# Kernel optimization log

Hardware: AMD Instinct MI355X
Metric: run time of the kernel (lower is better)

Reference implementation:

```python
import jax, jax.numpy as jnp
import numpy as np

B, L, H, NH = 8, 256, 128, 4
D = H // NH
NEG = jnp.float32(-(2.0 ** 32) + 1.0)


def setup_inputs() -> dict:
    key = jax.random.key(0)
    ks = jax.random.split(key, 12)
    f = lambda k, s, sc=1.0: jax.random.normal(k, s, dtype=jnp.float32) * sc
    inp = {
        "queries": f(ks[0], (B, L, H)),
        "keys": f(ks[1], (B, L, H)),
        "time_matrix_K": f(ks[2], (B, L, L, H), 0.05),
        "time_matrix_V": f(ks[3], (B, L, L, H), 0.05),
        "abs_pos_K": f(ks[4], (B, L, H), 0.1),
        "abs_pos_V": f(ks[5], (B, L, H), 0.1),
        "Wq": f(ks[6], (H, H), 1.0 / np.sqrt(H)),
        "bq": jnp.zeros((H,), jnp.float32),
        "Wk": f(ks[7], (H, H), 1.0 / np.sqrt(H)),
        "bk": jnp.zeros((H,), jnp.float32),
        "Wv": f(ks[8], (H, H), 1.0 / np.sqrt(H)),
        "bv": jnp.zeros((H,), jnp.float32),
        # True = padded query row (masked out)
        "time_mask": jax.random.uniform(ks[9], (B, L)) < 0.1,
        # causal mask: True above the diagonal = not attendable
        "attn_mask": jnp.triu(jnp.ones((L, L), dtype=bool), k=1),
    }
    return inp


def reference(queries, keys, time_matrix_K, time_matrix_V, abs_pos_K, abs_pos_V,
              Wq, bq, Wk, bk, Wv, bv, time_mask, attn_mask):
    # Linear projections (torch Linear: x @ W.T + b)
    Q = queries @ Wq.T + bq
    K = keys @ Wk.T + bk
    V = keys @ Wv.T + bv
    # head split: channels [i*D:(i+1)*D] -> head i  (equivalent to torch split/cat)
    Qh = Q.reshape(B, L, NH, D)
    Kh = K.reshape(B, L, NH, D)
    Vh = V.reshape(B, L, NH, D)
    pKh = abs_pos_K.reshape(B, L, NH, D)
    pVh = abs_pos_V.reshape(B, L, NH, D)
    tKh = time_matrix_K.reshape(B, L, L, NH, D)
    tVh = time_matrix_V.reshape(B, L, L, NH, D)
    # scores: QK^T + Q*absposK^T + per-row time-interval bias  -> [B,NH,L,L]
    aw = jnp.einsum('blhd,bmhd->bhlm', Qh, Kh)
    aw += jnp.einsum('blhd,bmhd->bhlm', Qh, pKh)
    aw += jnp.einsum('blmhd,blhd->bhlm', tKh, Qh)
    aw = aw * jnp.float32(1.0 / np.sqrt(D))
    mask = time_mask[:, None, :, None] | attn_mask[None, None, :, :]
    aw = jnp.where(mask, NEG, aw)
    A = jax.nn.softmax(aw, axis=-1)  # dropout omitted (eval mode)
    # outputs: A@V + A@absposV + per-row A @ time_matrix_V  -> [B,L,NH,D]
    out = jnp.einsum('bhlm,bmhd->blhd', A, Vh)
    out += jnp.einsum('bhlm,bmhd->blhd', A, pVh)
    out += jnp.einsum('bhlm,blmhd->blhd', A, tVh)
    return out.reshape(B, L, H)
```

## Files before the change

kernel.cpp:

```cpp
#include <hip/hip_runtime.h>
#include <math.h>

#define Bdim 8
#define Lq   256
#define Hd   128

static constexpr float kNEG = -4294967295.0f;
static constexpr float kScale = 0.17677669529663687f;
static constexpr float kUni = 0.00390625f;

__global__ __launch_bounds__(256) void prep_kernel(
    const float* __restrict__ Wq, const float* __restrict__ Wk,
    const float* __restrict__ Wv, const unsigned char* __restrict__ raw,
    float* __restrict__ Wt, int* __restrict__ outmask)
{
    const int blk = blockIdx.x;
    if (blk < 12) {
        __shared__ float tile[64][65];
        const int mi = blk >> 2;
        const float* W = (mi == 0) ? Wq : (mi == 1) ? Wk : Wv;
        float* WT = Wt + mi * (Hd * Hd);
        const int ti = blk & 3;
        const int r0 = (ti >> 1) * 64, c0 = (ti & 1) * 64;
        #pragma unroll
        for (int k = 0; k < 16; ++k) {
            const int e = threadIdx.x + k * 256;
            const int r = e >> 6, c = e & 63;
            tile[r][c] = W[(r0 + r) * Hd + (c0 + c)];
        }
        __syncthreads();
        #pragma unroll
        for (int k = 0; k < 16; ++k) {
            const int e = threadIdx.x + k * 256;
            const int r = e >> 6, c = e & 63;
            WT[(c0 + r) * Hd + (r0 + c)] = tile[c][r];
        }
    } else {
        __shared__ int cnt;
        if (threadIdx.x == 0) cnt = 0;
        __syncthreads();
        const int n = Bdim * Lq;
        for (int i = threadIdx.x; i < n; i += 256)
            if ((i & 3) && raw[i]) atomicAdd(&cnt, 1);
        __syncthreads();
        const bool is_u8 = (cnt > 0);
        const int* raw32 = (const int*)raw;
        for (int i = threadIdx.x; i < n; i += 256) {
            const int v = is_u8 ? (int)raw[i] : raw32[i];
            outmask[i] = (v != 0) ? 1 : 0;
        }
    }
}

__global__ __launch_bounds__(512) void proj_kernel(
    const float* __restrict__ queries, const float* __restrict__ keys,
    const float* __restrict__ absK, const float* __restrict__ absV,
    const float* __restrict__ Wt,
    const float* __restrict__ bq, const float* __restrict__ bk,
    const float* __restrict__ bv,
    float* __restrict__ Qb, float* __restrict__ Kb, float* __restrict__ Vb)
{
    constexpr int R = 8;
    __shared__ float xq[R][Hd];
    __shared__ float xk[R][Hd];
    const int row0 = blockIdx.x * R;
    const int tid = threadIdx.x;
    #pragma unroll
    for (int k = 0; k < 2; ++k) {
        const int e = tid + k * 512;
        const int r = e >> 7, c = e & 127;
        xq[r][c] = queries[(row0 + r) * Hd + c];
        xk[r][c] = keys[(row0 + r) * Hd + c];
    }
    __syncthreads();

    const int o = tid & 127, rh = tid >> 7;
    const int r0 = rh * 2, r1 = rh * 2 + 1;
    const float* __restrict__ Wtq = Wt;
    const float* __restrict__ Wtk = Wt + Hd * Hd;
    const float* __restrict__ Wtv = Wt + 2 * Hd * Hd;

    float qa0 = bq[o], qa1 = qa0;
    float ka0 = bk[o] + absK[(row0 + r0) * Hd + o];
    float ka1 = bk[o] + absK[(row0 + r1) * Hd + o];
    float va0 = bv[o] + absV[(row0 + r0) * Hd + o];
    float va1 = bv[o] + absV[(row0 + r1) * Hd + o];

    #pragma unroll 4
    for (int i = 0; i < Hd; ++i) {
        const float wq = Wtq[i * Hd + o];
        const float wk = Wtk[i * Hd + o];
        const float wv = Wtv[i * Hd + o];
        const float x0 = xq[r0][i], x1 = xq[r1][i];
        const float y0 = xk[r0][i], y1 = xk[r1][i];
        qa0 += x0 * wq; qa1 += x1 * wq;
        ka0 += y0 * wk; ka1 += y1 * wk;
        va0 += y0 * wv; va1 += y1 * wv;
    }
    Qb[(row0 + r0) * Hd + o] = qa0;  Qb[(row0 + r1) * Hd + o] = qa1;
    Kb[(row0 + r0) * Hd + o] = ka0;  Kb[(row0 + r1) * Hd + o] = ka1;
    Vb[(row0 + r0) * Hd + o] = va0;  Vb[(row0 + r1) * Hd + o] = va1;
}

__global__ __launch_bounds__(256) void attn_kernel(
    const float* __restrict__ Qb, const float* __restrict__ Kb,
    const float* __restrict__ Vb,
    const float* __restrict__ tK, const float* __restrict__ tV,
    const int* __restrict__ tmask, float* __restrict__ out)
{
    const int bid = blockIdx.x;
    const int b  = bid & 7;
    const int hp = (bid >> 3) & 1;
    const int j  = bid >> 4;

    const int tid = threadIdx.x;
    const int w = tid >> 6;
    const int h = hp * 2 + (w & 1);
    const int p = j * 2 + (w >> 1);
    const int l0 = p;
    const int l1 = 255 - p;
    const int m_off = (tid >> 2) & 15;
    const int cg = tid & 3;
    const int ch = h * 32 + cg * 8;

    const float* q0b = Qb + ((size_t)b * Lq + l0) * Hd + ch;
    const float* q1b = Qb + ((size_t)b * Lq + l1) * Hd + ch;
    float4 q00 = ((const float4*)q0b)[0], q01 = ((const float4*)q0b)[1];
    float4 q10 = ((const float4*)q1b)[0], q11 = ((const float4*)q1b)[1];
    q00.x*=kScale; q00.y*=kScale; q00.z*=kScale; q00.w*=kScale;
    q01.x*=kScale; q01.y*=kScale; q01.z*=kScale; q01.w*=kScale;
    q10.x*=kScale; q10.y*=kScale; q10.z*=kScale; q10.w*=kScale;
    q11.x*=kScale; q11.y*=kScale; q11.z*=kScale; q11.w*=kScale;

    const bool mk0 = (tmask[b * Lq + l0] != 0);
    const bool mk1 = (tmask[b * Lq + l1] != 0);
    const int ntc0 = (l0 >> 4) + 1, ntc1 = (l1 >> 4) + 1;
    const int n10 = mk0 ? 0 : ntc0, n11 = mk1 ? 0 : ntc1;
    const int NT1 = (n10 > n11) ? n10 : n11;
    const int n20 = mk0 ? 16 : ntc0, n21 = mk1 ? 16 : ntc1;
    const int NT2 = (n20 > n21) ? n20 : n21;

    const float* kpt = Kb + (size_t)b * Lq * Hd + m_off * Hd + ch;
    const float* vpt = Vb + (size_t)b * Lq * Hd + m_off * Hd + ch;
    const float* t0p = tK + (((size_t)b * Lq + l0) * Lq + m_off) * Hd + ch;
    const float* t1p = tK + (((size_t)b * Lq + l1) * Lq + m_off) * Hd + ch;
    const float* u0p = tV + (((size_t)b * Lq + l0) * Lq + m_off) * Hd + ch;
    const float* u1p = tV + (((size_t)b * Lq + l1) * Lq + m_off) * Hd + ch;

    float s0[16], s1[16];
    #pragma unroll
    for (int t = 0; t < 16; ++t) { s0[t] = kNEG; s1[t] = kNEG; }

    #pragma unroll
    for (int t = 0; t < 16; ++t) {
        if (t < NT1) {
            const float4 ka = *(const float4*)(kpt + t * 2048);
            const float4 kb = *(const float4*)(kpt + t * 2048 + 4);
            const int m = t * 16 + m_off;
            if (t < n10) {
                const float4 ta = *(const float4*)(t0p + t * 2048);
                const float4 tb = *(const float4*)(t0p + t * 2048 + 4);
                float pp = q00.x*(ka.x+ta.x) + q00.y*(ka.y+ta.y)
                         + q00.z*(ka.z+ta.z) + q00.w*(ka.w+ta.w)
                         + q01.x*(kb.x+tb.x) + q01.y*(kb.y+tb.y)
                         + q01.z*(kb.z+tb.z) + q01.w*(kb.w+tb.w);
                pp += __shfl_xor(pp, 1);
                pp += __shfl_xor(pp, 2);
                s0[t] = (m <= l0) ? pp : kNEG;
            }
            if (t < n11) {
                const float4 ta = *(const float4*)(t1p + t * 2048);
                const float4 tb = *(const float4*)(t1p + t * 2048 + 4);
                float pp = q10.x*(ka.x+ta.x) + q10.y*(ka.y+ta.y)
                         + q10.z*(ka.z+ta.z) + q10.w*(ka.w+ta.w)
                         + q11.x*(kb.x+tb.x) + q11.y*(kb.y+tb.y)
                         + q11.z*(kb.z+tb.z) + q11.w*(kb.w+tb.w);
                pp += __shfl_xor(pp, 1);
                pp += __shfl_xor(pp, 2);
                s1[t] = (m <= l1) ? pp : kNEG;
            }
        }
    }

    if (!mk0) {
        float mx = s0[0];
        #pragma unroll
        for (int t = 1; t < 16; ++t) mx = fmaxf(mx, s0[t]);
        #pragma unroll
        for (int d = 4; d < 64; d <<= 1) mx = fmaxf(mx, __shfl_xor(mx, d));
        float sum = 0.f;
        #pragma unroll
        for (int t = 0; t < 16; ++t) { s0[t] = expf(s0[t] - mx); sum += s0[t]; }
        #pragma unroll
        for (int d = 4; d < 64; d <<= 1) sum += __shfl_xor(sum, d);
        const float inv = 1.0f / sum;
        #pragma unroll
        for (int t = 0; t < 16; ++t) s0[t] *= inv;
    } else {
        #pragma unroll
        for (int t = 0; t < 16; ++t) s0[t] = kUni;
    }
    if (!mk1) {
        float mx = s1[0];
        #pragma unroll
        for (int t = 1; t < 16; ++t) mx = fmaxf(mx, s1[t]);
        #pragma unroll
        for (int d = 4; d < 64; d <<= 1) mx = fmaxf(mx, __shfl_xor(mx, d));
        float sum = 0.f;
        #pragma unroll
        for (int t = 0; t < 16; ++t) { s1[t] = expf(s1[t] - mx); sum += s1[t]; }
        #pragma unroll
        for (int d = 4; d < 64; d <<= 1) sum += __shfl_xor(sum, d);
        const float inv = 1.0f / sum;
        #pragma unroll
        for (int t = 0; t < 16; ++t) s1[t] *= inv;
    } else {
        #pragma unroll
        for (int t = 0; t < 16; ++t) s1[t] = kUni;
    }

    float4 a00 = {0,0,0,0}, a01 = {0,0,0,0};
    float4 a10 = {0,0,0,0}, a11 = {0,0,0,0};
    #pragma unroll
    for (int t = 0; t < 16; ++t) {
        if (t < NT2) {
            const float4 va = *(const float4*)(vpt + t * 2048);
            const float4 vb = *(const float4*)(vpt + t * 2048 + 4);
            if (t < n20) {
                const float4 ta = *(const float4*)(u0p + t * 2048);
                const float4 tb = *(const float4*)(u0p + t * 2048 + 4);
                const float aw = s0[t];
                a00.x += aw*(va.x+ta.x); a00.y += aw*(va.y+ta.y);
                a00.z += aw*(va.z+ta.z); a00.w += aw*(va.w+ta.w);
                a01.x += aw*(vb.x+tb.x); a01.y += aw*(vb.y+tb.y);
                a01.z += aw*(vb.z+tb.z); a01.w += aw*(vb.w+tb.w);
            }
            if (t < n21) {
                const float4 ta = *(const float4*)(u1p + t * 2048);
                const float4 tb = *(const float4*)(u1p + t * 2048 + 4);
                const float aw = s1[t];
                a10.x += aw*(va.x+ta.x); a10.y += aw*(va.y+ta.y);
                a10.z += aw*(va.z+ta.z); a10.w += aw*(va.w+ta.w);
                a11.x += aw*(vb.x+tb.x); a11.y += aw*(vb.y+tb.y);
                a11.z += aw*(vb.z+tb.z); a11.w += aw*(vb.w+tb.w);
            }
        }
    }
    #pragma unroll
    for (int d = 4; d < 64; d <<= 1) {
        a00.x += __shfl_xor(a00.x, d); a00.y += __shfl_xor(a00.y, d);
        a00.z += __shfl_xor(a00.z, d); a00.w += __shfl_xor(a00.w, d);
        a01.x += __shfl_xor(a01.x, d); a01.y += __shfl_xor(a01.y, d);
        a01.z += __shfl_xor(a01.z, d); a01.w += __shfl_xor(a01.w, d);
        a10.x += __shfl_xor(a10.x, d); a10.y += __shfl_xor(a10.y, d);
        a10.z += __shfl_xor(a10.z, d); a10.w += __shfl_xor(a10.w, d);
        a11.x += __shfl_xor(a11.x, d); a11.y += __shfl_xor(a11.y, d);
        a11.z += __shfl_xor(a11.z, d); a11.w += __shfl_xor(a11.w, d);
    }
    if (m_off == 0) {
        float* o0 = out + ((size_t)b * Lq + l0) * Hd + ch;
        ((float4*)o0)[0] = a00; ((float4*)o0)[1] = a01;
        float* o1 = out + ((size_t)b * Lq + l1) * Hd + ch;
        ((float4*)o1)[0] = a10; ((float4*)o1)[1] = a11;
    }
}

extern "C" void kernel_launch(void* const* d_in, const int* in_sizes, int n_in,
                              void* d_out, int out_size, void* d_ws, size_t ws_size,
                              hipStream_t stream) {
    const float* queries = (const float*)d_in[0];
    const float* keys    = (const float*)d_in[1];
    const float* tK      = (const float*)d_in[2];
    const float* tV      = (const float*)d_in[3];
    const float* absK    = (const float*)d_in[4];
    const float* absV    = (const float*)d_in[5];
    const float* Wq      = (const float*)d_in[6];
    const float* bq      = (const float*)d_in[7];
    const float* Wk      = (const float*)d_in[8];
    const float* bk      = (const float*)d_in[9];
    const float* Wv      = (const float*)d_in[10];
    const float* bv      = (const float*)d_in[11];
    const unsigned char* tmask_raw = (const unsigned char*)d_in[12];

    float* outp = (float*)d_out;

    const int rows = Bdim * Lq;
    float* Qb = (float*)d_ws;
    float* Kb = Qb + (size_t)rows * Hd;
    float* Vb = Kb + (size_t)rows * Hd;
    int* tmask = (int*)(Vb + (size_t)rows * Hd);
    float* Wt = (float*)(tmask + rows);

    prep_kernel<<<13, 256, 0, stream>>>(Wq, Wk, Wv, tmask_raw, Wt, tmask);
    proj_kernel<<<rows / 8, 512, 0, stream>>>(queries, keys, absK, absV, Wt,
                                              bq, bk, bv, Qb, Kb, Vb);
    attn_kernel<<<1024, 256, 0, stream>>>(Qb, Kb, Vb, tK, tV, tmask, outp);
}
```

Measured before the change: 77.50 us.

## Assign one row pair per block across all heads with LDS softmax

Each block now handles one (l0, l1) query-row pair for all four heads instead of two heads across two row pairs. Lanes are remapped so a wave reads full 512-byte rows of the time matrices, and the m tiles are split across waves. Scores are staged in shared memory, softmax runs one head per wave, and per-wave partial outputs are reduced through shared memory. This is meant to improve coalescing and wave load balance on the dominant time-matrix reads, at the cost of extra barriers and LDS traffic, plus a launch-bounds occupancy hint.

```diff
diff --git a/kernel.cpp b/kernel.cpp
--- a/kernel.cpp
+++ b/kernel.cpp
@@ -102,31 +102,34 @@
     Vb[(row0 + r0) * Hd + o] = va0;  Vb[(row0 + r1) * Hd + o] = va1;
 }
 
-__global__ __launch_bounds__(256) void attn_kernel(
+__global__ __launch_bounds__(256, 4) void attn_kernel(
     const float* __restrict__ Qb, const float* __restrict__ Kb,
     const float* __restrict__ Vb,
     const float* __restrict__ tK, const float* __restrict__ tV,
     const int* __restrict__ tmask, float* __restrict__ out)
 {
     const int bid = blockIdx.x;
-    const int b  = bid & 7;
-    const int hp = (bid >> 3) & 1;
-    const int j  = bid >> 4;
+    const int b = bid & 7;
+    const int p = bid >> 3;
+    const int l0 = p, l1 = 255 - p;
 
     const int tid = threadIdx.x;
     const int w = tid >> 6;
-    const int h = hp * 2 + (w & 1);
-    const int p = j * 2 + (w >> 1);
-    const int l0 = p;
-    const int l1 = 255 - p;
-    const int m_off = (tid >> 2) & 15;
-    const int cg = tid & 3;
-    const int ch = h * 32 + cg * 8;
-
-    const float* q0b = Qb + ((size_t)b * Lq + l0) * Hd + ch;
-    const float* q1b = Qb + ((size_t)b * Lq + l1) * Hd + ch;
-    float4 q00 = ((const float4*)q0b)[0], q01 = ((const float4*)q0b)[1];
-    float4 q10 = ((const float4*)q1b)[0], q11 = ((const float4*)q1b)[1];
+    const int lane = tid & 63;
+    const int cg = lane & 15;
+    const int mo = lane >> 4;
+    const int hq = cg >> 2;
+
+    __shared__ float sc[2][4][264];
+    __shared__ float op[4][2][128];
+
+    const size_t row0 = ((size_t)b * Lq + l0) * Hd;
+    const size_t row1 = ((size_t)b * Lq + l1) * Hd;
+
+    float4 q00 = *(const float4*)(Qb + row0 + cg * 8);
+    float4 q01 = *(const float4*)(Qb + row0 + cg * 8 + 4);
+    float4 q10 = *(const float4*)(Qb + row1 + cg * 8);
+    float4 q11 = *(const float4*)(Qb + row1 + cg * 8 + 4);
     q00.x*=kScale; q00.y*=kScale; q00.z*=kScale; q00.w*=kScale;
     q01.x*=kScale; q01.y*=kScale; q01.z*=kScale; q01.w*=kScale;
     q10.x*=kScale; q10.y*=kScale; q10.z*=kScale; q10.w*=kScale;
@@ -140,105 +143,112 @@
     const int n20 = mk0 ? 16 : ntc0, n21 = mk1 ? 16 : ntc1;
     const int NT2 = (n20 > n21) ? n20 : n21;
 
-    const float* kpt = Kb + (size_t)b * Lq * Hd + m_off * Hd + ch;
-    const float* vpt = Vb + (size_t)b * Lq * Hd + m_off * Hd + ch;
-    const float* t0p = tK + (((size_t)b * Lq + l0) * Lq + m_off) * Hd + ch;
-    const float* t1p = tK + (((size_t)b * Lq + l1) * Lq + m_off) * Hd + ch;
-    const float* u0p = tV + (((size_t)b * Lq + l0) * Lq + m_off) * Hd + ch;
-    const float* u1p = tV + (((size_t)b * Lq + l1) * Lq + m_off) * Hd + ch;
-
-    float s0[16], s1[16];
-    #pragma unroll
-    for (int t = 0; t < 16; ++t) { s0[t] = kNEG; s1[t] = kNEG; }
-
-    #pragma unroll
-    for (int t = 0; t < 16; ++t) {
-        if (t < NT1) {
-            const float4 ka = *(const float4*)(kpt + t * 2048);
-            const float4 kb = *(const float4*)(kpt + t * 2048 + 4);
-            const int m = t * 16 + m_off;
+    const float* kp  = Kb + (size_t)b * Lq * Hd + (size_t)mo * Hd + cg * 8;
+    const float* vp  = Vb + (size_t)b * Lq * Hd + (size_t)mo * Hd + cg * 8;
+    const float* t0p = tK + row0 * Lq + (size_t)mo * Hd + cg * 8;
+    const float* t1p = tK + row1 * Lq + (size_t)mo * Hd + cg * 8;
+    const float* u0p = tV + row0 * Lq + (size_t)mo * Hd + cg * 8;
+    const float* u1p = tV + row1 * Lq + (size_t)mo * Hd + cg * 8;
+
+    for (int k = 0; k < 4; ++k) {
+        const int t = w + k * 4;
+        if (t >= NT1) break;
+        #pragma unroll
+        for (int sub = 0; sub < 4; ++sub) {
+            const int off = t * 2048 + sub * 512;
+            const int m = t * 16 + sub * 4 + mo;
+            const float4 ka = *(const float4*)(kp + off);
+            const float4 kb = *(const float4*)(kp + off + 4);
             if (t < n10) {
-                const float4 ta = *(const float4*)(t0p + t * 2048);
-                const float4 tb = *(const float4*)(t0p + t * 2048 + 4);
+                const float4 ta = *(const float4*)(t0p + off);
+                const float4 tb = *(const float4*)(t0p + off + 4);
                 float pp = q00.x*(ka.x+ta.x) + q00.y*(ka.y+ta.y)
                          + q00.z*(ka.z+ta.z) + q00.w*(ka.w+ta.w)
                          + q01.x*(kb.x+tb.x) + q01.y*(kb.y+tb.y)
                          + q01.z*(kb.z+tb.z) + q01.w*(kb.w+tb.w);
                 pp += __shfl_xor(pp, 1);
                 pp += __shfl_xor(pp, 2);
-                s0[t] = (m <= l0) ? pp : kNEG;
+                if ((lane & 3) == 0) sc[0][hq][m] = (m <= l0) ? pp : kNEG;
             }
             if (t < n11) {
-                const float4 ta = *(const float4*)(t1p + t * 2048);
-                const float4 tb = *(const float4*)(t1p + t * 2048 + 4);
+                const float4 ta = *(const float4*)(t1p + off);
+                const float4 tb = *(const float4*)(t1p + off + 4);
                 float pp = q10.x*(ka.x+ta.x) + q10.y*(ka.y+ta.y)
                          + q10.z*(ka.z+ta.z) + q10.w*(ka.w+ta.w)
                          + q11.x*(kb.x+tb.x) + q11.y*(kb.y+tb.y)
                          + q11.z*(kb.z+tb.z) + q11.w*(kb.w+tb.w);
                 pp += __shfl_xor(pp, 1);
                 pp += __shfl_xor(pp, 2);
-                s1[t] = (m <= l1) ? pp : kNEG;
+                if ((lane & 3) == 0) sc[1][hq][m] = (m <= l1) ? pp : kNEG;
             }
         }
     }
+    __syncthreads();
 
     if (!mk0) {
-        float mx = s0[0];
-        #pragma unroll
-        for (int t = 1; t < 16; ++t) mx = fmaxf(mx, s0[t]);
-        #pragma unroll
-        for (int d = 4; d < 64; d <<= 1) mx = fmaxf(mx, __shfl_xor(mx, d));
-        float sum = 0.f;
-        #pragma unroll
-        for (int t = 0; t < 16; ++t) { s0[t] = expf(s0[t] - mx); sum += s0[t]; }
-        #pragma unroll
-        for (int d = 4; d < 64; d <<= 1) sum += __shfl_xor(sum, d);
+        float v0 = (lane       <= l0) ? sc[0][w][lane]       : kNEG;
+        float v1 = (lane + 64  <= l0) ? sc[0][w][lane + 64]  : kNEG;
+        float v2 = (lane + 128 <= l0) ? sc[0][w][lane + 128] : kNEG;
+        float v3 = (lane + 192 <= l0) ? sc[0][w][lane + 192] : kNEG;
+        float mx = fmaxf(fmaxf(v0, v1), fmaxf(v2, v3));
+        #pragma unroll
+        for (int d = 1; d < 64; d <<= 1) mx = fmaxf(mx, __shfl_xor(mx, d));
+        v0 = expf(v0 - mx); v1 = expf(v1 - mx);
+        v2 = expf(v2 - mx); v3 = expf(v3 - mx);
+        float sum = v0 + v1 + v2 + v3;
+        #pragma unroll
+        for (int d = 1; d < 64; d <<= 1) sum += __shfl_xor(sum, d);
         const float inv = 1.0f / sum;
-        #pragma unroll
-        for (int t = 0; t < 16; ++t) s0[t] *= inv;
-    } else {
-        #pragma unroll
-        for (int t = 0; t < 16; ++t) s0[t] = kUni;
+        sc[0][w][lane]       = v0 * inv;
+        sc[0][w][lane + 64]  = v1 * inv;
+        sc[0][w][lane + 128] = v2 * inv;
+        sc[0][w][lane + 192] = v3 * inv;
     }
     if (!mk1) {
-        float mx = s1[0];
-        #pragma unroll
-        for (int t = 1; t < 16; ++t) mx = fmaxf(mx, s1[t]);
-        #pragma unroll
-        for (int d = 4; d < 64; d <<= 1) mx = fmaxf(mx, __shfl_xor(mx, d));
-        float sum = 0.f;
-        #pragma unroll
-        for (int t = 0; t < 16; ++t) { s1[t] = expf(s1[t] - mx); sum += s1[t]; }
-        #pragma unroll
-        for (int d = 4; d < 64; d <<= 1) sum += __shfl_xor(sum, d);
+        float v0 = (lane       <= l1) ? sc[1][w][lane]       : kNEG;
+        float v1 = (lane + 64  <= l1) ? sc[1][w][lane + 64]  : kNEG;
+        float v2 = (lane + 128 <= l1) ? sc[1][w][lane + 128] : kNEG;
+        float v3 = (lane + 192 <= l1) ? sc[1][w][lane + 192] : kNEG;
+        float mx = fmaxf(fmaxf(v0, v1), fmaxf(v2, v3));
+        #pragma unroll
+        for (int d = 1; d < 64; d <<= 1) mx = fmaxf(mx, __shfl_xor(mx, d));
+        v0 = expf(v0 - mx); v1 = expf(v1 - mx);
+        v2 = expf(v2 - mx); v3 = expf(v3 - mx);
+        float sum = v0 + v1 + v2 + v3;
+        #pragma unroll
+        for (int d = 1; d < 64; d <<= 1) sum += __shfl_xor(sum, d);
         const float inv = 1.0f / sum;
-        #pragma unroll
-        for (int t = 0; t < 16; ++t) s1[t] *= inv;
-    } else {
-        #pragma unroll
-        for (int t = 0; t < 16; ++t) s1[t] = kUni;
-    }
+        sc[1][w][lane]       = v0 * inv;
+        sc[1][w][lane + 64]  = v1 * inv;
+        sc[1][w][lane + 128] = v2 * inv;
+        sc[1][w][lane + 192] = v3 * inv;
+    }
+    __syncthreads();
 
     float4 a00 = {0,0,0,0}, a01 = {0,0,0,0};
     float4 a10 = {0,0,0,0}, a11 = {0,0,0,0};
-    #pragma unroll
-    for (int t = 0; t < 16; ++t) {
-        if (t < NT2) {
-            const float4 va = *(const float4*)(vpt + t * 2048);
-            const float4 vb = *(const float4*)(vpt + t * 2048 + 4);
+    for (int k = 0; k < 4; ++k) {
+        const int t = w + k * 4;
+        if (t >= NT2) break;
+        #pragma unroll
+        for (int sub = 0; sub < 4; ++sub) {
+            const int off = t * 2048 + sub * 512;
+            const int m = t * 16 + sub * 4 + mo;
+            const float4 va = *(const float4*)(vp + off);
+            const float4 vb = *(const float4*)(vp + off + 4);
             if (t < n20) {
-                const float4 ta = *(const float4*)(u0p + t * 2048);
-                const float4 tb = *(const float4*)(u0p + t * 2048 + 4);
-                const float aw = s0[t];
+                const float aw = mk0 ? kUni : sc[0][hq][m];
+                const float4 ta = *(const float4*)(u0p + off);
+                const float4 tb = *(const float4*)(u0p + off + 4);
                 a00.x += aw*(va.x+ta.x); a00.y += aw*(va.y+ta.y);
                 a00.z += aw*(va.z+ta.z); a00.w += aw*(va.w+ta.w);
                 a01.x += aw*(vb.x+tb.x); a01.y += aw*(vb.y+tb.y);
                 a01.z += aw*(vb.z+tb.z); a01.w += aw*(vb.w+tb.w);
             }
             if (t < n21) {
-                const float4 ta = *(const float4*)(u1p + t * 2048);
-                const float4 tb = *(const float4*)(u1p + t * 2048 + 4);
-                const float aw = s1[t];
+                const float aw = mk1 ? kUni : sc[1][hq][m];
+                const float4 ta = *(const float4*)(u1p + off);
+                const float4 tb = *(const float4*)(u1p + off + 4);
                 a10.x += aw*(va.x+ta.x); a10.y += aw*(va.y+ta.y);
                 a10.z += aw*(va.z+ta.z); a10.w += aw*(va.w+ta.w);
                 a11.x += aw*(vb.x+tb.x); a11.y += aw*(vb.y+tb.y);
@@ -247,7 +257,7 @@
         }
     }
     #pragma unroll
-    for (int d = 4; d < 64; d <<= 1) {
+    for (int d = 16; d < 64; d <<= 1) {
         a00.x += __shfl_xor(a00.x, d); a00.y += __shfl_xor(a00.y, d);
         a00.z += __shfl_xor(a00.z, d); a00.w += __shfl_xor(a00.w, d);
         a01.x += __shfl_xor(a01.x, d); a01.y += __shfl_xor(a01.y, d);
@@ -257,11 +267,19 @@
         a11.x += __shfl_xor(a11.x, d); a11.y += __shfl_xor(a11.y, d);
         a11.z += __shfl_xor(a11.z, d); a11.w += __shfl_xor(a11.w, d);
     }
-    if (m_off == 0) {
-        float* o0 = out + ((size_t)b * Lq + l0) * Hd + ch;
-        ((float4*)o0)[0] = a00; ((float4*)o0)[1] = a01;
-        float* o1 = out + ((size_t)b * Lq + l1) * Hd + ch;
-        ((float4*)o1)[0] = a10; ((float4*)o1)[1] = a11;
+    if (mo == 0) {
+        *(float4*)&op[w][0][cg * 8]     = a00;
+        *(float4*)&op[w][0][cg * 8 + 4] = a01;
+        *(float4*)&op[w][1][cg * 8]     = a10;
+        *(float4*)&op[w][1][cg * 8 + 4] = a11;
+    }
+    __syncthreads();
+
+    {
+        const int li = tid >> 7, ch = tid & 127;
+        const float s = op[0][li][ch] + op[1][li][ch]
+                      + op[2][li][ch] + op[3][li][ch];
+        out[(li ? row1 : row0) + ch] = s;
     }
 }
 
```

Result: no change. 78.30 us (+1.0%).
